# Kernel tuning notes

Hardware: AMD Instinct MI355X
Metric: run time of the kernel (lower is better)

Reference implementation:

```python
import jax, jax.numpy as jnp
import numpy as np

B, S, E, N, H = 2, 2048, 2048, 16, 128  # batch, seq, embed, heads, depth


def sine_table(features, length, min_timescale=1.0, max_timescale=10000.0):
    fraction = jnp.arange(0, features, 2, dtype=jnp.float32) / features
    timescale = min_timescale * (max_timescale / min_timescale) ** fraction
    sinusoid_inp = jnp.einsum('i,j->ij', jnp.arange(length, dtype=jnp.float32), 1.0 / timescale,
                              precision=jax.lax.Precision.HIGHEST)
    sinusoid_inp = jnp.concatenate([sinusoid_inp, sinusoid_inp], axis=-1)  # [L, features]
    return jnp.sin(sinusoid_inp), jnp.cos(sinusoid_inp)


def rotate_half(x):
    x1, x2 = jnp.split(x, 2, axis=-1)
    return jnp.concatenate([-x2, x1], axis=-1)


def apply_rotary(q, k, cos, sin):
    # q: [B,S,N,H], k: [B,T,N,H]; cos/sin: [L,H] broadcast over (seq, depth)
    qcos = cos[: q.shape[1]][None, :, None, :]
    qsin = sin[: q.shape[1]][None, :, None, :]
    kcos = cos[: k.shape[1]][None, :, None, :]
    ksin = sin[: k.shape[1]][None, :, None, :]
    return q * qcos + rotate_half(q) * qsin, k * kcos + rotate_half(k) * ksin


def setup_inputs() -> dict:
    key = jax.random.key(0)
    ks = jax.random.split(key, 6)
    scale = 1.0 / np.sqrt(E)
    return {
        'x_q': jax.random.normal(ks[0], (B, S, E), jnp.float32),
        'x_kv': jax.random.normal(ks[1], (B, S, E), jnp.float32),
        'WQ': jax.random.normal(ks[2], (E, N, H), jnp.float32) * scale,
        'WK': jax.random.normal(ks[3], (E, N, H), jnp.float32) * scale,
        'WV': jax.random.normal(ks[4], (E, N, H), jnp.float32) * scale,
        'WO': jax.random.normal(ks[5], (N, H, E), jnp.float32) * scale,
    }


def reference(x_q, x_kv, WQ, WK, WV, WO):
    q = jnp.einsum('bse,enh->bsnh', x_q, WQ)
    k = jnp.einsum('bte,enh->btnh', x_kv, WK)
    v = jnp.einsum('bte,enh->btnh', x_kv, WV)

    sin, cos = sine_table(q.shape[-1], max(q.shape[1], k.shape[1]))
    q, k = apply_rotary(q, k, cos, sin)

    # causal attention bias: [1,1,S,T]
    s_len, t_len = q.shape[1], k.shape[1]
    causal = jnp.arange(s_len)[:, None] >= jnp.arange(t_len)[None, :]
    bias = jnp.where(causal, 0.0, -1e10).astype(jnp.float32)[None, None]

    logits = jnp.einsum('bsnh,btnh->bnst', q, k) / np.sqrt(H) + bias
    probs = jax.nn.softmax(logits, axis=-1)
    a = jnp.einsum('bnst,btnh->bsnh', probs, v)
    o = jnp.einsum('bsnh,nhe->bse', a, WO)
    return o
```

## Files before the change

### kernel.cpp

```cpp
#include <hip/hip_runtime.h>
#include <hip/hip_bf16.h>

typedef __bf16 bf16;
typedef __attribute__((ext_vector_type(8))) __bf16 bf16x8;
typedef __attribute__((ext_vector_type(4))) __bf16 bf16x4;
typedef __attribute__((ext_vector_type(4))) float f32x4;

typedef const __attribute__((address_space(1))) void* gptr_t;
typedef __attribute__((address_space(3))) void* sptr_t;

__device__ __forceinline__ void gload16(const void* g, void* l) {
  __builtin_amdgcn_global_load_lds((gptr_t)g, (sptr_t)l, 16, 0, 0);
}

#define MFMA_BF16(a, b, c) __builtin_amdgcn_mfma_f32_16x16x32_bf16((a), (b), (c), 0, 0, 0)

#define BAR() do { asm volatile("" ::: "memory"); __builtin_amdgcn_s_barrier(); asm volatile("" ::: "memory"); } while (0)

__device__ __forceinline__ int swzb(int l) { return l ^ (((l >> 7) & 7) << 4); }

namespace {
constexpr int kB = 2, kS = 2048, kE = 2048, kN = 16, kH = 128;
constexpr float kScale = 0.08838834764831845f;
constexpr float kLog2e = 1.4426950408889634f;
}

__global__ void k_cvt(const float* __restrict__ in, bf16* __restrict__ out) {
  int i = blockIdx.x * 256 + threadIdx.x;
  float4 v = reinterpret_cast<const float4*>(in)[i];
  bf16x4 o = { (bf16)v.x, (bf16)v.y, (bf16)v.z, (bf16)v.w };
  reinterpret_cast<bf16x4*>(out)[i] = o;
}

__global__ void k_tconv(const float* __restrict__ in, bf16* __restrict__ out) {
  __shared__ bf16 tile[64][66];
  int bx = blockIdx.x & 31, by = blockIdx.x >> 5;
  int r0 = by * 64, c0 = bx * 64;
  int t = threadIdx.x;
  int c = t & 63, rb = t >> 6;
#pragma unroll
  for (int j = 0; j < 16; ++j) {
    int r = rb + j * 4;
    tile[r][c] = (bf16)in[(size_t)(r0 + r) * 2048 + c0 + c];
  }
  __syncthreads();
  int rr = t & 63;
#pragma unroll
  for (int j = 0; j < 16; ++j) {
    int cc = rb + j * 4;
    out[(size_t)(c0 + cc) * 2048 + r0 + rr] = tile[rr][cc];
  }
}

__global__ void k_vtrans(const bf16* __restrict__ V, bf16* __restrict__ Vt) {
  __shared__ bf16 tile[64][66];
  int bid = blockIdx.x;
  int bn = bid >> 6;
  int s0 = ((bid >> 1) & 31) * 64;
  int h0 = (bid & 1) * 64;
  size_t base = (size_t)bn * kS * kH;
  int t = threadIdx.x, c = t & 63, rb = t >> 6;
#pragma unroll
  for (int j = 0; j < 16; ++j) {
    int r = rb + j * 4;
    tile[r][c] = V[base + (size_t)(s0 + r) * kH + h0 + c];
  }
  __syncthreads();
#pragma unroll
  for (int j = 0; j < 16; ++j) {
    int hh = rb + j * 4;
    Vt[base + (size_t)(h0 + hh) * kS + s0 + (t & 63)] = tile[t & 63][hh];
  }
}

__global__ void k_trig(float* __restrict__ ctab, float* __restrict__ stab) {
  int tid = blockIdx.x * 256 + threadIdx.x;
  int s = tid >> 6, i = tid & 63;
  float inv = exp2f(-(float)i * 0.20762050593046457f);
  float ang = (float)s * inv;
  float sn, cs;
  sincosf(ang, &sn, &cs);
  ctab[tid] = cs;
  stab[tid] = sn;
}

__global__ void k_rope(bf16* __restrict__ Qd, bf16* __restrict__ Kd,
                       const float* __restrict__ ctab, const float* __restrict__ stab) {
  int tid = blockIdx.x * 256 + threadIdx.x;
  int i = tid & 63;
  int s = (tid >> 6) & (kS - 1);
  int bn = tid >> 17;
  size_t base = ((size_t)bn * kS + s) * kH;
  float cs = ctab[(s << 6) + i], sn = stab[(s << 6) + i];
  float q1 = (float)Qd[base + i], q2 = (float)Qd[base + i + 64];
  Qd[base + i]      = (bf16)(q1 * cs - q2 * sn);
  Qd[base + i + 64] = (bf16)(q2 * cs + q1 * sn);
  float k1 = (float)Kd[base + i], k2 = (float)Kd[base + i + 64];
  Kd[base + i]      = (bf16)(k1 * cs - k2 * sn);
  Kd[base + i + 64] = (bf16)(k2 * cs + k1 * sn);
}


__device__ __forceinline__ void stage_half(const bf16* __restrict__ src, size_t row0,
                                           int k0, char* slot, int t) {
#pragma unroll
  for (int i = 0; i < 2; ++i) {
    int idx = i * 512 + t;
    int d = idx * 16;
    int lb = d ^ (((d >> 7) & 7) << 4);
    int r = lb >> 7;
    int kc = (lb & 127) >> 1;
    gload16(src + (row0 + r) * 2048 + k0 + kc,
            slot + i * 8192 + (t >> 6) * 1024);
  }
}

#define ASB(b, h) ((char*)LDS + (b) * 32768 + (h) * 16384)
#define BSB(b, h) ((char*)LDS + 65536 + (b) * 32768 + (h) * 16384)
#define AS1(b)    ((char*)LDS + (b) * 16384)
#define BS1(q, h) ((char*)LDS + 32768 + (q) * 32768 + (h) * 16384)

template <int MODE>
__global__ __launch_bounds__(512, 2) void k_gemm8(const bf16* __restrict__ Aq,
                                                  const bf16* __restrict__ Akv,
                                                  const bf16* __restrict__ Bt,
                                                  void* __restrict__ Cout) {
  constexpr int NTN = (MODE == 0) ? 24 : 8;
  constexpr int NTM = (MODE == 0) ? 16 : 32;
  constexpr int NT = 32;
  constexpr int BM = (MODE == 0) ? 256 : 128;
  __shared__ __align__(16) char LDS[131072];
  int bid = blockIdx.x;
  constexpr int nblk = NTM * NTN;
  int swz = (bid & 7) * (nblk >> 3) + (bid >> 3);
  int mt = swz / NTN, nt = swz - mt * NTN;
  size_t m0 = (size_t)mt * BM;
  int n0 = nt * 256;
  const bf16* A = (MODE == 0 && nt >= 8) ? Akv : Aq;
  int t = threadIdx.x, wid = t >> 6, lane = t & 63;
  int l16 = lane & 15, lq = lane >> 4;
  int wr = wid >> 2, wc = wid & 3;
  int bhalf = wc >> 1;
  int brow0 = ((wc & 1) << 6) + l16;

  constexpr int MF = (MODE == 0) ? 8 : 4;
  f32x4 acc[MF][4] = {};
  bf16x8 af[4], bfr[4];

  if constexpr (MODE == 0) {
    stage_half(Bt, (size_t)n0,       0, BSB(0, 0), t);
    stage_half(Bt, (size_t)n0 + 128, 0, BSB(0, 1), t);
    stage_half(A,  m0,               0, ASB(0, 0), t);
    stage_half(A,  m0 + 128,         0, ASB(0, 1), t);
    stage_half(Bt, (size_t)n0,      64, BSB(1, 0), t);
    stage_half(Bt, (size_t)n0 + 128, 64, BSB(1, 1), t);
    asm volatile("s_waitcnt vmcnt(4)" ::: "memory");
    BAR();

    for (int kt = 0; kt < NT; ++kt) {
      int buf = kt & 1, nbuf = buf ^ 1;
#pragma unroll
      for (int j = 0; j < 4; ++j) {
        int l = ((j * 16 + l16) << 7) + (lq << 4);
        af[j] = *(const bf16x8*)(ASB(buf, wr) + swzb(l));
      }
#pragma unroll
      for (int nf = 0; nf < 4; ++nf) {
        int l = ((brow0 + nf * 16) << 7) + (lq << 4);
        bfr[nf] = *(const bf16x8*)(BSB(buf, bhalf) + swzb(l));
      }
      if (kt + 1 < NT) stage_half(A, m0, (kt + 1) * 64, ASB(nbuf, 0), t);
      BAR();
      __builtin_amdgcn_s_setprio(1);
#pragma unroll
      for (int j = 0; j < 4; ++j)
#pragma unroll
        for (int nf = 0; nf < 4; ++nf)
          acc[j][nf] = MFMA_BF16(af[j], bfr[nf], acc[j][nf]);
      __builtin_amdgcn_s_setprio(0);
      BAR();
#pragma unroll
      for (int j = 0; j < 4; ++j) {
        int l = (((j + 4) * 16 + l16) << 7) + (lq << 4);
        af[j] = *(const bf16x8*)(ASB(buf, wr) + swzb(l));
      }
      if (kt + 1 < NT) stage_half(A, m0 + 128, (kt + 1) * 64, ASB(nbuf, 1), t);
      BAR();
      __builtin_amdgcn_s_setprio(1);
#pragma unroll
      for (int j = 0; j < 4; ++j)
#pragma unroll
        for (int nf = 0; nf < 4; ++nf)
          acc[j + 4][nf] = MFMA_BF16(af[j], bfr[nf], acc[j + 4][nf]);
      __builtin_amdgcn_s_setprio(0);
      BAR();
#pragma unroll
      for (int j = 0; j < 4; ++j) {
        int l = ((j * 16 + l16) << 7) + 64 + (lq << 4);
        af[j] = *(const bf16x8*)(ASB(buf, wr) + swzb(l));
      }
#pragma unroll
      for (int nf = 0; nf < 4; ++nf) {
        int l = ((brow0 + nf * 16) << 7) + 64 + (lq << 4);
        bfr[nf] = *(const bf16x8*)(BSB(buf, bhalf) + swzb(l));
      }
      BAR();
      __builtin_amdgcn_s_setprio(1);
#pragma unroll
      for (int j = 0; j < 4; ++j)
#pragma unroll
        for (int nf = 0; nf < 4; ++nf)
          acc[j][nf] = MFMA_BF16(af[j], bfr[nf], acc[j][nf]);
      __builtin_amdgcn_s_setprio(0);
      BAR();
#pragma unroll
      for (int j = 0; j < 4; ++j) {
        int l = (((j + 4) * 16 + l16) << 7) + 64 + (lq << 4);
        af[j] = *(const bf16x8*)(ASB(buf, wr) + swzb(l));
      }
      if (kt + 2 < NT) {
        stage_half(Bt, (size_t)n0,       (kt + 2) * 64, BSB(buf, 0), t);
        stage_half(Bt, (size_t)n0 + 128, (kt + 2) * 64, BSB(buf, 1), t);
      }
      BAR();
      __builtin_amdgcn_s_setprio(1);
#pragma unroll
      for (int j = 0; j < 4; ++j)
#pragma unroll
        for (int nf = 0; nf < 4; ++nf)
          acc[j + 4][nf] = MFMA_BF16(af[j], bfr[nf], acc[j + 4][nf]);
      __builtin_amdgcn_s_setprio(0);
      if (kt < NT - 2)       asm volatile("s_waitcnt vmcnt(4)" ::: "memory");
      else if (kt == NT - 2) asm volatile("s_waitcnt vmcnt(0)" ::: "memory");
      BAR();
    }
  } else {
    stage_half(Bt, (size_t)n0,       0, BS1(0, 0), t);
    stage_half(Bt, (size_t)n0 + 128, 0, BS1(0, 1), t);
    stage_half(A,  m0,               0, AS1(0), t);
    stage_half(Bt, (size_t)n0,      64, BS1(1, 0), t);
    stage_half(Bt, (size_t)n0 + 128, 64, BS1(1, 1), t);
    asm volatile("s_waitcnt vmcnt(4)" ::: "memory");
    BAR();

    int bql = 0;
    for (int kt = 0; kt < NT; ++kt) {
      char* Ab = AS1(kt & 1);
      char* Anb = AS1((kt & 1) ^ 1);
      char* Bb = BS1(bql, bhalf);
      int bq2 = bql + 2; if (bq2 >= 3) bq2 -= 3;
#pragma unroll
      for (int j = 0; j < 4; ++j) {
        int l = (((wr * 4 + j) * 16 + l16) << 7) + (lq << 4);
        af[j] = *(const bf16x8*)(Ab + swzb(l));
      }
#pragma unroll
      for (int nf = 0; nf < 2; ++nf) {
        int l = ((brow0 + nf * 16) << 7) + (lq << 4);
        bfr[nf] = *(const bf16x8*)(Bb + swzb(l));
      }
      if (kt + 1 < NT) stage_half(A, m0, (kt + 1) * 64, Anb, t);
      BAR();
      __builtin_amdgcn_s_setprio(1);
#pragma unroll
      for (int j = 0; j < 4; ++j)
#pragma unroll
        for (int nf = 0; nf < 2; ++nf)
          acc[j][nf] = MFMA_BF16(af[j], bfr[nf], acc[j][nf]);
      __builtin_amdgcn_s_setprio(0);
      BAR();
#pragma unroll
      for (int nf = 0; nf < 2; ++nf) {
        int l = ((brow0 + (nf + 2) * 16) << 7) + (lq << 4);
        bfr[2 + nf] = *(const bf16x8*)(Bb + swzb(l));
      }
      if (kt + 2 < NT) {
        stage_half(Bt, (size_t)n0,       (kt + 2) * 64, BS1(bq2, 0), t);
        stage_half(Bt, (size_t)n0 + 128, (kt + 2) * 64, BS1(bq2, 1), t);
      }
      BAR();
      __builtin_amdgcn_s_setprio(1);
#pragma unroll
      for (int j = 0; j < 4; ++j)
#pragma unroll
        for (int nf = 0; nf < 2; ++nf)
          acc[j][2 + nf] = MFMA_BF16(af[j], bfr[2 + nf], acc[j][2 + nf]);
      __builtin_amdgcn_s_setprio(0);
      BAR();
#pragma unroll
      for (int j = 0; j < 4; ++j) {
        int l = (((wr * 4 + j) * 16 + l16) << 7) + 64 + (lq << 4);
        af[j] = *(const bf16x8*)(Ab + swzb(l));
      }
#pragma unroll
      for (int nf = 0; nf < 2; ++nf) {
        int l = ((brow0 + nf * 16) << 7) + 64 + (lq << 4);
        bfr[nf] = *(const bf16x8*)(Bb + swzb(l));
      }
      BAR();
      __builtin_amdgcn_s_setprio(1);
#pragma unroll
      for (int j = 0; j < 4; ++j)
#pragma unroll
        for (int nf = 0; nf < 2; ++nf)
          acc[j][nf] = MFMA_BF16(af[j], bfr[nf], acc[j][nf]);
      __builtin_amdgcn_s_setprio(0);
      BAR();
#pragma unroll
      for (int nf = 0; nf < 2; ++nf) {
        int l = ((brow0 + (nf + 2) * 16) << 7) + 64 + (lq << 4);
        bfr[2 + nf] = *(const bf16x8*)(Bb + swzb(l));
      }
      BAR();
      __builtin_amdgcn_s_setprio(1);
#pragma unroll
      for (int j = 0; j < 4; ++j)
#pragma unroll
        for (int nf = 0; nf < 2; ++nf)
          acc[j][2 + nf] = MFMA_BF16(af[j], bfr[2 + nf], acc[j][2 + nf]);
      __builtin_amdgcn_s_setprio(0);
      if (kt < NT - 2)       asm volatile("s_waitcnt vmcnt(4)" ::: "memory");
      else if (kt == NT - 2) asm volatile("s_waitcnt vmcnt(0)" ::: "memory");
      BAR();
      bql += 1; if (bql >= 3) bql -= 3;
    }
  }

  constexpr int WRS = (MODE == 0) ? 128 : 64;
#pragma unroll
  for (int mf = 0; mf < MF; ++mf) {
    int rowb = (int)m0 + wr * WRS + mf * 16 + lq * 4;
#pragma unroll
    for (int nf = 0; nf < 4; ++nf) {
      int col = n0 + wc * 64 + nf * 16 + l16;
#pragma unroll
      for (int r = 0; r < 4; ++r) {
        float v = acc[mf][nf][r];
        int mrow = rowb + r;
        if (MODE == 0) {
          int grp = col >> 11, cw = col & 2047;
          int b = mrow >> 11, s = mrow & 2047, n = cw >> 7, h = cw & 127;
          ((bf16*)Cout)[(size_t)grp * 8388608 +
                        (((size_t)(b * 16 + n) * 2048 + s) << 7) + h] = (bf16)v;
        } else {
          ((float*)Cout)[((size_t)mrow << 11) + col] = v;
        }
      }
    }
  }
}

__global__ __launch_bounds__(512, 4) void k_attn(const bf16* __restrict__ Q,
                                                 const bf16* __restrict__ Kg,
                                                 const bf16* __restrict__ Vt,
                                                 bf16* __restrict__ AO) {
  __shared__ __align__(16) bf16 Ks[64 * 128];
  __shared__ __align__(16) bf16 Vs[128 * 64];
  __shared__ __align__(16) bf16 Ps[8][16][72];
  int bid = blockIdx.x;
  int half = bid >> 8;
  int bn = (half << 4) | ((bid >> 4) & 15);
  int qt = (bid & 15) ^ (half ? 15 : 0);
  int q0 = qt * 128;
  int t = threadIdx.x, wid = t >> 6, lane = t & 63;
  int l16 = lane & 15, lq = lane >> 4;
  size_t bnSH = (size_t)bn * kS * kH;

  int qrow_a = q0 + wid * 16 + l16;
  bf16x8 qf[4];
#pragma unroll
  for (int ks = 0; ks < 4; ++ks)
    qf[ks] = *(const bf16x8*)(Q + bnSH + (size_t)qrow_a * kH + ks * 32 + lq * 8);

  f32x4 oacc[8] = {};
  float mrun[4], lrun[4];
#pragma unroll
  for (int r = 0; r < 4; ++r) { mrun[r] = -1e30f; lrun[r] = 0.f; }

  int ntiles = (q0 + 128) >> 6;
  for (int kt = 0; kt < ntiles; ++kt) {
    int kv0 = kt * 64;
#pragma unroll
    for (int i = 0; i < 2; ++i) {
      int idx = i * 512 + t;
      {
        int row = idx >> 4, ch = idx & 15;
        int gch = ch ^ (row & 7);
        gload16(Kg + bnSH + (size_t)(kv0 + row) * kH + gch * 8,
                (char*)Ks + i * 8192 + wid * 1024);
      }
      {
        int row = idx >> 3, ch = idx & 7;
        int gch = ch ^ (row & 7);
        gload16(Vt + bnSH + (size_t)row * kS + kv0 + gch * 8,
                (char*)Vs + i * 8192 + wid * 1024);
      }
    }
    __syncthreads();

    f32x4 sacc[4] = {};
#pragma unroll
    for (int ks = 0; ks < 4; ++ks) {
#pragma unroll
      for (int ni = 0; ni < 4; ++ni) {
        int sp = ni * 16 + l16;
        int hb = (ks * 32 + lq * 8) * 2;
        bf16x8 kb = *(const bf16x8*)((const char*)Ks + sp * 256 + (hb ^ ((sp & 7) << 4)));
        sacc[ni] = MFMA_BF16(qf[ks], kb, sacc[ni]);
      }
    }

    bool need_mask = (kv0 + 63) > (q0 + wid * 16);
#pragma unroll
    for (int ni = 0; ni < 4; ++ni) {
      f32x4 v = sacc[ni] * kScale;
      if (need_mask) {
#pragma unroll
        for (int r = 0; r < 4; ++r) {
          int qrow = q0 + wid * 16 + lq * 4 + r;
          int col = kv0 + ni * 16 + l16;
          if (col > qrow) v[r] = -1e30f;
        }
      }
      sacc[ni] = v;
    }

#pragma unroll
    for (int r = 0; r < 4; ++r) {
      float pm = fmaxf(fmaxf(sacc[0][r], sacc[1][r]),
                       fmaxf(sacc[2][r], sacc[3][r]));
      pm = fmaxf(pm, __shfl_xor(pm, 1));
      pm = fmaxf(pm, __shfl_xor(pm, 2));
      pm = fmaxf(pm, __shfl_xor(pm, 4));
      pm = fmaxf(pm, __shfl_xor(pm, 8));
      float mold = mrun[r];
      float mnew = fmaxf(mold, pm);
      float alpha = exp2f((mold - mnew) * kLog2e);
      mrun[r] = mnew;
      float rs = 0.f;
#pragma unroll
      for (int ni = 0; ni < 4; ++ni) {
        float p = exp2f((sacc[ni][r] - mnew) * kLog2e);
        sacc[ni][r] = p;
        rs += p;
      }
      rs += __shfl_xor(rs, 1);
      rs += __shfl_xor(rs, 2);
      rs += __shfl_xor(rs, 4);
      rs += __shfl_xor(rs, 8);
      lrun[r] = lrun[r] * alpha + rs;
#pragma unroll
      for (int nj = 0; nj < 8; ++nj) oacc[nj][r] *= alpha;
    }

#pragma unroll
    for (int ni = 0; ni < 4; ++ni)
#pragma unroll
      for (int r = 0; r < 4; ++r)
        Ps[wid][lq * 4 + r][ni * 16 + l16] = (bf16)sacc[ni][r];

#pragma unroll
    for (int ks = 0; ks < 2; ++ks) {
      bf16x8 pa = *(const bf16x8*)&Ps[wid][l16][ks * 32 + lq * 8];
#pragma unroll
      for (int nj = 0; nj < 8; ++nj) {
        int h = nj * 16 + l16;
        int sb = (ks * 64 + lq * 16) ^ ((h & 7) << 4);
        bf16x8 vb = *(const bf16x8*)((const char*)Vs + h * 128 + sb);
        oacc[nj] = MFMA_BF16(pa, vb, oacc[nj]);
      }
    }
    __syncthreads();
  }

  int b = bn >> 4, n = bn & 15;
#pragma unroll
  for (int r = 0; r < 4; ++r) {
    float inv = 1.0f / lrun[r];
    int qrow = q0 + wid * 16 + lq * 4 + r;
#pragma unroll
    for (int nj = 0; nj < 8; ++nj) {
      float v = oacc[nj][r] * inv;
      AO[(((size_t)b * kS + qrow) * kN + n) * kH + nj * 16 + l16] = (bf16)v;
    }
  }
}

extern "C" void kernel_launch(void* const* d_in, const int* in_sizes, int n_in,
                              void* d_out, int out_size, void* d_ws, size_t ws_size,
                              hipStream_t stream) {
  (void)in_sizes; (void)n_in; (void)out_size; (void)ws_size;
  const float* x_q  = (const float*)d_in[0];
  const float* x_kv = (const float*)d_in[1];
  const float* WQ   = (const float*)d_in[2];
  const float* WK   = (const float*)d_in[3];
  const float* WV   = (const float*)d_in[4];
  const float* WO   = (const float*)d_in[5];
  float* out = (float*)d_out;
  char* w = (char*)d_ws;
  const size_t MB = 1ull << 20;
  bf16* xq  = (bf16*)(w + 0 * MB);
  bf16* xkv = (bf16*)(w + 16 * MB);
  bf16* WqT = (bf16*)(w + 32 * MB);
  bf16* WkT = (bf16*)(w + 40 * MB);
  bf16* WvT = (bf16*)(w + 48 * MB);
  bf16* WoT = (bf16*)(w + 56 * MB);
  bf16* Qb  = (bf16*)(w + 64 * MB);
  bf16* Kb  = (bf16*)(w + 80 * MB);
  bf16* Vb  = (bf16*)(w + 96 * MB);
  float* ctab = (float*)(w + 0 * MB);
  float* stab = (float*)(w + 1 * MB);
  bf16* AO  = xq;
  bf16* Vtb = xkv;

  k_cvt<<<8192, 256, 0, stream>>>(x_q, xq);
  k_cvt<<<8192, 256, 0, stream>>>(x_kv, xkv);
  k_tconv<<<1024, 256, 0, stream>>>(WQ, WqT);
  k_tconv<<<1024, 256, 0, stream>>>(WK, WkT);
  k_tconv<<<1024, 256, 0, stream>>>(WV, WvT);
  k_tconv<<<1024, 256, 0, stream>>>(WO, WoT);
  k_gemm8<0><<<384, 512, 0, stream>>>(xq, xkv, WqT, Qb);
  k_trig<<<512, 256, 0, stream>>>(ctab, stab);
  k_rope<<<16384, 256, 0, stream>>>(Qb, Kb, ctab, stab);
  k_vtrans<<<2048, 256, 0, stream>>>(Vb, Vtb);
  k_attn<<<512, 512, 0, stream>>>(Qb, Kb, Vtb, AO);
  k_gemm8<1><<<256, 512, 0, stream>>>(AO, AO, WoT, out);
}
```

Baseline: 447.6 us.

## Merge prep kernels, vectorize transposes and rope, unify GEMM to 128-row tiles

Two conversion launches become one, and the four weight-transpose launches become one. The transpose, V-transpose and rope kernels now use 8-wide bf16 and float4 vector loads and stores in place of scalar element accesses. The QKV projection GEMM drops its 256-row tile path and reuses the 128-row triple-buffered-B path with twice as many blocks. The attention P staging buffer gets an XOR swizzle in place of padding, to avoid LDS bank conflicts. These changes aim to cut launch overhead and memory-instruction count, at the cost of more A-tile reloads per B tile in the projection GEMM.

```diff
diff --git a/kernel.cpp b/kernel.cpp
--- a/kernel.cpp
+++ b/kernel.cpp
@@ -25,51 +25,73 @@
 constexpr float kLog2e = 1.4426950408889634f;
 }
 
-__global__ void k_cvt(const float* __restrict__ in, bf16* __restrict__ out) {
-  int i = blockIdx.x * 256 + threadIdx.x;
+__global__ void k_cvt2(const float* __restrict__ a, const float* __restrict__ b,
+                       bf16* __restrict__ oa, bf16* __restrict__ ob) {
+  int bid = blockIdx.x;
+  const float* in = (bid < 8192) ? a : b;
+  bf16* out = (bid < 8192) ? oa : ob;
+  int i = (bid & 8191) * 256 + threadIdx.x;
   float4 v = reinterpret_cast<const float4*>(in)[i];
   bf16x4 o = { (bf16)v.x, (bf16)v.y, (bf16)v.z, (bf16)v.w };
   reinterpret_cast<bf16x4*>(out)[i] = o;
 }
 
-__global__ void k_tconv(const float* __restrict__ in, bf16* __restrict__ out) {
-  __shared__ bf16 tile[64][66];
-  int bx = blockIdx.x & 31, by = blockIdx.x >> 5;
+__global__ void k_tconv4(const float* __restrict__ WQ, const float* __restrict__ WK,
+                         const float* __restrict__ WV, const float* __restrict__ WO,
+                         bf16* __restrict__ OQ, bf16* __restrict__ OK2,
+                         bf16* __restrict__ OV, bf16* __restrict__ OO) {
+  __shared__ float tile[64][68];
+  int bid = blockIdx.x;
+  int sel = bid >> 10;
+  const float* in = (sel == 0) ? WQ : (sel == 1) ? WK : (sel == 2) ? WV : WO;
+  bf16* out = (sel == 0) ? OQ : (sel == 1) ? OK2 : (sel == 2) ? OV : OO;
+  int lb = bid & 1023;
+  int bx = lb & 31, by = lb >> 5;
   int r0 = by * 64, c0 = bx * 64;
   int t = threadIdx.x;
-  int c = t & 63, rb = t >> 6;
-#pragma unroll
-  for (int j = 0; j < 16; ++j) {
-    int r = rb + j * 4;
-    tile[r][c] = (bf16)in[(size_t)(r0 + r) * 2048 + c0 + c];
+  int rr = t >> 4, c4 = (t & 15) * 4;
+#pragma unroll
+  for (int k = 0; k < 4; ++k) {
+    int r = rr + k * 16;
+    float4 v = *reinterpret_cast<const float4*>(&in[(size_t)(r0 + r) * 2048 + c0 + c4]);
+    tile[r][c4] = v.x; tile[r][c4 + 1] = v.y; tile[r][c4 + 2] = v.z; tile[r][c4 + 3] = v.w;
   }
   __syncthreads();
-  int rr = t & 63;
-#pragma unroll
-  for (int j = 0; j < 16; ++j) {
-    int cc = rb + j * 4;
-    out[(size_t)(c0 + cc) * 2048 + r0 + rr] = tile[rr][cc];
+  int cc0 = t >> 3, r8 = (t & 7) * 8;
+#pragma unroll
+  for (int k = 0; k < 2; ++k) {
+    int cc = cc0 + k * 32;
+    bf16x8 o;
+#pragma unroll
+    for (int j = 0; j < 8; ++j) o[j] = (bf16)tile[r8 + j][cc];
+    *reinterpret_cast<bf16x8*>(&out[(size_t)(c0 + cc) * 2048 + r0 + r8]) = o;
   }
 }
 
 __global__ void k_vtrans(const bf16* __restrict__ V, bf16* __restrict__ Vt) {
-  __shared__ bf16 tile[64][66];
+  __shared__ bf16 tile[64][72];
   int bid = blockIdx.x;
   int bn = bid >> 6;
   int s0 = ((bid >> 1) & 31) * 64;
   int h0 = (bid & 1) * 64;
   size_t base = (size_t)bn * kS * kH;
-  int t = threadIdx.x, c = t & 63, rb = t >> 6;
-#pragma unroll
-  for (int j = 0; j < 16; ++j) {
-    int r = rb + j * 4;
-    tile[r][c] = V[base + (size_t)(s0 + r) * kH + h0 + c];
+  int t = threadIdx.x;
+  int r = t >> 3, c8 = (t & 7) * 8;
+#pragma unroll
+  for (int k = 0; k < 2; ++k) {
+    int rr = r + k * 32;
+    *reinterpret_cast<bf16x8*>(&tile[rr][c8]) =
+        *reinterpret_cast<const bf16x8*>(&V[base + (size_t)(s0 + rr) * kH + h0 + c8]);
   }
   __syncthreads();
-#pragma unroll
-  for (int j = 0; j < 16; ++j) {
-    int hh = rb + j * 4;
-    Vt[base + (size_t)(h0 + hh) * kS + s0 + (t & 63)] = tile[t & 63][hh];
+  int hh0 = t >> 3, s8 = (t & 7) * 8;
+#pragma unroll
+  for (int k = 0; k < 2; ++k) {
+    int hh = hh0 + k * 32;
+    bf16x8 o;
+#pragma unroll
+    for (int j = 0; j < 8; ++j) o[j] = tile[s8 + j][hh];
+    *reinterpret_cast<bf16x8*>(&Vt[base + (size_t)(h0 + hh) * kS + s0 + s8]) = o;
   }
 }
 
@@ -87,17 +109,34 @@
 __global__ void k_rope(bf16* __restrict__ Qd, bf16* __restrict__ Kd,
                        const float* __restrict__ ctab, const float* __restrict__ stab) {
   int tid = blockIdx.x * 256 + threadIdx.x;
-  int i = tid & 63;
-  int s = (tid >> 6) & (kS - 1);
-  int bn = tid >> 17;
+  int i8 = (tid & 7) * 8;
+  int s = (tid >> 3) & (kS - 1);
+  int bn = tid >> 14;
   size_t base = ((size_t)bn * kS + s) * kH;
-  float cs = ctab[(s << 6) + i], sn = stab[(s << 6) + i];
-  float q1 = (float)Qd[base + i], q2 = (float)Qd[base + i + 64];
-  Qd[base + i]      = (bf16)(q1 * cs - q2 * sn);
-  Qd[base + i + 64] = (bf16)(q2 * cs + q1 * sn);
-  float k1 = (float)Kd[base + i], k2 = (float)Kd[base + i + 64];
-  Kd[base + i]      = (bf16)(k1 * cs - k2 * sn);
-  Kd[base + i + 64] = (bf16)(k2 * cs + k1 * sn);
+  float4 c0 = *reinterpret_cast<const float4*>(&ctab[(s << 6) + i8]);
+  float4 c1 = *reinterpret_cast<const float4*>(&ctab[(s << 6) + i8 + 4]);
+  float4 s0 = *reinterpret_cast<const float4*>(&stab[(s << 6) + i8]);
+  float4 s1 = *reinterpret_cast<const float4*>(&stab[(s << 6) + i8 + 4]);
+  float cs[8] = {c0.x, c0.y, c0.z, c0.w, c1.x, c1.y, c1.z, c1.w};
+  float sn[8] = {s0.x, s0.y, s0.z, s0.w, s1.x, s1.y, s1.z, s1.w};
+  bf16x8 qlo = *reinterpret_cast<const bf16x8*>(&Qd[base + i8]);
+  bf16x8 qhi = *reinterpret_cast<const bf16x8*>(&Qd[base + 64 + i8]);
+  bf16x8 klo = *reinterpret_cast<const bf16x8*>(&Kd[base + i8]);
+  bf16x8 khi = *reinterpret_cast<const bf16x8*>(&Kd[base + 64 + i8]);
+  bf16x8 qlo2, qhi2, klo2, khi2;
+#pragma unroll
+  for (int j = 0; j < 8; ++j) {
+    float q1 = (float)qlo[j], q2 = (float)qhi[j];
+    qlo2[j] = (bf16)(q1 * cs[j] - q2 * sn[j]);
+    qhi2[j] = (bf16)(q2 * cs[j] + q1 * sn[j]);
+    float k1 = (float)klo[j], k2 = (float)khi[j];
+    klo2[j] = (bf16)(k1 * cs[j] - k2 * sn[j]);
+    khi2[j] = (bf16)(k2 * cs[j] + k1 * sn[j]);
+  }
+  *reinterpret_cast<bf16x8*>(&Qd[base + i8]) = qlo2;
+  *reinterpret_cast<bf16x8*>(&Qd[base + 64 + i8]) = qhi2;
+  *reinterpret_cast<bf16x8*>(&Kd[base + i8]) = klo2;
+  *reinterpret_cast<bf16x8*>(&Kd[base + 64 + i8]) = khi2;
 }
 
 
@@ -115,8 +154,6 @@
   }
 }
 
-#define ASB(b, h) ((char*)LDS + (b) * 32768 + (h) * 16384)
-#define BSB(b, h) ((char*)LDS + 65536 + (b) * 32768 + (h) * 16384)
 #define AS1(b)    ((char*)LDS + (b) * 16384)
 #define BS1(q, h) ((char*)LDS + 32768 + (q) * 32768 + (h) * 16384)
 
@@ -126,15 +163,14 @@
                                                   const bf16* __restrict__ Bt,
                                                   void* __restrict__ Cout) {
   constexpr int NTN = (MODE == 0) ? 24 : 8;
-  constexpr int NTM = (MODE == 0) ? 16 : 32;
+  constexpr int NTM = 32;
   constexpr int NT = 32;
-  constexpr int BM = (MODE == 0) ? 256 : 128;
   __shared__ __align__(16) char LDS[131072];
   int bid = blockIdx.x;
   constexpr int nblk = NTM * NTN;
   int swz = (bid & 7) * (nblk >> 3) + (bid >> 3);
   int mt = swz / NTN, nt = swz - mt * NTN;
-  size_t m0 = (size_t)mt * BM;
+  size_t m0 = (size_t)mt * 128;
   int n0 = nt * 256;
   const bf16* A = (MODE == 0 && nt >= 8) ? Akv : Aq;
   int t = threadIdx.x, wid = t >> 6, lane = t & 63;
@@ -143,193 +179,102 @@
   int bhalf = wc >> 1;
   int brow0 = ((wc & 1) << 6) + l16;
 
-  constexpr int MF = (MODE == 0) ? 8 : 4;
-  f32x4 acc[MF][4] = {};
+  f32x4 acc[4][4] = {};
   bf16x8 af[4], bfr[4];
 
-  if constexpr (MODE == 0) {
-    stage_half(Bt, (size_t)n0,       0, BSB(0, 0), t);
-    stage_half(Bt, (size_t)n0 + 128, 0, BSB(0, 1), t);
-    stage_half(A,  m0,               0, ASB(0, 0), t);
-    stage_half(A,  m0 + 128,         0, ASB(0, 1), t);
-    stage_half(Bt, (size_t)n0,      64, BSB(1, 0), t);
-    stage_half(Bt, (size_t)n0 + 128, 64, BSB(1, 1), t);
-    asm volatile("s_waitcnt vmcnt(4)" ::: "memory");
-    BAR();
-
-    for (int kt = 0; kt < NT; ++kt) {
-      int buf = kt & 1, nbuf = buf ^ 1;
-#pragma unroll
-      for (int j = 0; j < 4; ++j) {
-        int l = ((j * 16 + l16) << 7) + (lq << 4);
-        af[j] = *(const bf16x8*)(ASB(buf, wr) + swzb(l));
-      }
-#pragma unroll
-      for (int nf = 0; nf < 4; ++nf) {
-        int l = ((brow0 + nf * 16) << 7) + (lq << 4);
-        bfr[nf] = *(const bf16x8*)(BSB(buf, bhalf) + swzb(l));
-      }
-      if (kt + 1 < NT) stage_half(A, m0, (kt + 1) * 64, ASB(nbuf, 0), t);
-      BAR();
-      __builtin_amdgcn_s_setprio(1);
-#pragma unroll
-      for (int j = 0; j < 4; ++j)
-#pragma unroll
-        for (int nf = 0; nf < 4; ++nf)
-          acc[j][nf] = MFMA_BF16(af[j], bfr[nf], acc[j][nf]);
-      __builtin_amdgcn_s_setprio(0);
-      BAR();
-#pragma unroll
-      for (int j = 0; j < 4; ++j) {
-        int l = (((j + 4) * 16 + l16) << 7) + (lq << 4);
-        af[j] = *(const bf16x8*)(ASB(buf, wr) + swzb(l));
-      }
-      if (kt + 1 < NT) stage_half(A, m0 + 128, (kt + 1) * 64, ASB(nbuf, 1), t);
-      BAR();
-      __builtin_amdgcn_s_setprio(1);
-#pragma unroll
-      for (int j = 0; j < 4; ++j)
-#pragma unroll
-        for (int nf = 0; nf < 4; ++nf)
-          acc[j + 4][nf] = MFMA_BF16(af[j], bfr[nf], acc[j + 4][nf]);
-      __builtin_amdgcn_s_setprio(0);
-      BAR();
-#pragma unroll
-      for (int j = 0; j < 4; ++j) {
-        int l = ((j * 16 + l16) << 7) + 64 + (lq << 4);
-        af[j] = *(const bf16x8*)(ASB(buf, wr) + swzb(l));
-      }
-#pragma unroll
-      for (int nf = 0; nf < 4; ++nf) {
-        int l = ((brow0 + nf * 16) << 7) + 64 + (lq << 4);
-        bfr[nf] = *(const bf16x8*)(BSB(buf, bhalf) + swzb(l));
-      }
-      BAR();
-      __builtin_amdgcn_s_setprio(1);
-#pragma unroll
-      for (int j = 0; j < 4; ++j)
-#pragma unroll
-        for (int nf = 0; nf < 4; ++nf)
-          acc[j][nf] = MFMA_BF16(af[j], bfr[nf], acc[j][nf]);
-      __builtin_amdgcn_s_setprio(0);
-      BAR();
-#pragma unroll
-      for (int j = 0; j < 4; ++j) {
-        int l = (((j + 4) * 16 + l16) << 7) + 64 + (lq << 4);
-        af[j] = *(const bf16x8*)(ASB(buf, wr) + swzb(l));
-      }
-      if (kt + 2 < NT) {
-        stage_half(Bt, (size_t)n0,       (kt + 2) * 64, BSB(buf, 0), t);
-        stage_half(Bt, (size_t)n0 + 128, (kt + 2) * 64, BSB(buf, 1), t);
-      }
-      BAR();
-      __builtin_amdgcn_s_setprio(1);
-#pragma unroll
-      for (int j = 0; j < 4; ++j)
-#pragma unroll
-        for (int nf = 0; nf < 4; ++nf)
-          acc[j + 4][nf] = MFMA_BF16(af[j], bfr[nf], acc[j + 4][nf]);
-      __builtin_amdgcn_s_setprio(0);
-      if (kt < NT - 2)       asm volatile("s_waitcnt vmcnt(4)" ::: "memory");
-      else if (kt == NT - 2) asm volatile("s_waitcnt vmcnt(0)" ::: "memory");
-      BAR();
-    }
-  } else {
-    stage_half(Bt, (size_t)n0,       0, BS1(0, 0), t);
-    stage_half(Bt, (size_t)n0 + 128, 0, BS1(0, 1), t);
-    stage_half(A,  m0,               0, AS1(0), t);
-    stage_half(Bt, (size_t)n0,      64, BS1(1, 0), t);
-    stage_half(Bt, (size_t)n0 + 128, 64, BS1(1, 1), t);
-    asm volatile("s_waitcnt vmcnt(4)" ::: "memory");
-    BAR();
-
-    int bql = 0;
-    for (int kt = 0; kt < NT; ++kt) {
-      char* Ab = AS1(kt & 1);
-      char* Anb = AS1((kt & 1) ^ 1);
-      char* Bb = BS1(bql, bhalf);
-      int bq2 = bql + 2; if (bq2 >= 3) bq2 -= 3;
-#pragma unroll
-      for (int j = 0; j < 4; ++j) {
-        int l = (((wr * 4 + j) * 16 + l16) << 7) + (lq << 4);
-        af[j] = *(const bf16x8*)(Ab + swzb(l));
-      }
-#pragma unroll
-      for (int nf = 0; nf < 2; ++nf) {
-        int l = ((brow0 + nf * 16) << 7) + (lq << 4);
-        bfr[nf] = *(const bf16x8*)(Bb + swzb(l));
-      }
-      if (kt + 1 < NT) stage_half(A, m0, (kt + 1) * 64, Anb, t);
-      BAR();
-      __builtin_amdgcn_s_setprio(1);
-#pragma unroll
-      for (int j = 0; j < 4; ++j)
-#pragma unroll
-        for (int nf = 0; nf < 2; ++nf)
-          acc[j][nf] = MFMA_BF16(af[j], bfr[nf], acc[j][nf]);
-      __builtin_amdgcn_s_setprio(0);
-      BAR();
-#pragma unroll
-      for (int nf = 0; nf < 2; ++nf) {
-        int l = ((brow0 + (nf + 2) * 16) << 7) + (lq << 4);
-        bfr[2 + nf] = *(const bf16x8*)(Bb + swzb(l));
-      }
-      if (kt + 2 < NT) {
-        stage_half(Bt, (size_t)n0,       (kt + 2) * 64, BS1(bq2, 0), t);
-        stage_half(Bt, (size_t)n0 + 128, (kt + 2) * 64, BS1(bq2, 1), t);
-      }
-      BAR();
-      __builtin_amdgcn_s_setprio(1);
-#pragma unroll
-      for (int j = 0; j < 4; ++j)
-#pragma unroll
-        for (int nf = 0; nf < 2; ++nf)
-          acc[j][2 + nf] = MFMA_BF16(af[j], bfr[2 + nf], acc[j][2 + nf]);
-      __builtin_amdgcn_s_setprio(0);
-      BAR();
-#pragma unroll
-      for (int j = 0; j < 4; ++j) {
-        int l = (((wr * 4 + j) * 16 + l16) << 7) + 64 + (lq << 4);
-        af[j] = *(const bf16x8*)(Ab + swzb(l));
-      }
-#pragma unroll
-      for (int nf = 0; nf < 2; ++nf) {
-        int l = ((brow0 + nf * 16) << 7) + 64 + (lq << 4);
-        bfr[nf] = *(const bf16x8*)(Bb + swzb(l));
-      }
-      BAR();
-      __builtin_amdgcn_s_setprio(1);
-#pragma unroll
-      for (int j = 0; j < 4; ++j)
-#pragma unroll
-        for (int nf = 0; nf < 2; ++nf)
-          acc[j][nf] = MFMA_BF16(af[j], bfr[nf], acc[j][nf]);
-      __builtin_amdgcn_s_setprio(0);
-      BAR();
-#pragma unroll
-      for (int nf = 0; nf < 2; ++nf) {
-        int l = ((brow0 + (nf + 2) * 16) << 7) + 64 + (lq << 4);
-        bfr[2 + nf] = *(const bf16x8*)(Bb + swzb(l));
-      }
-      BAR();
-      __builtin_amdgcn_s_setprio(1);
-#pragma unroll
-      for (int j = 0; j < 4; ++j)
-#pragma unroll
-        for (int nf = 0; nf < 2; ++nf)
-          acc[j][2 + nf] = MFMA_BF16(af[j], bfr[2 + nf], acc[j][2 + nf]);
-      __builtin_amdgcn_s_setprio(0);
-      if (kt < NT - 2)       asm volatile("s_waitcnt vmcnt(4)" ::: "memory");
-      else if (kt == NT - 2) asm volatile("s_waitcnt vmcnt(0)" ::: "memory");
-      BAR();
-      bql += 1; if (bql >= 3) bql -= 3;
-    }
-  }
-
-  constexpr int WRS = (MODE == 0) ? 128 : 64;
-#pragma unroll
-  for (int mf = 0; mf < MF; ++mf) {
-    int rowb = (int)m0 + wr * WRS + mf * 16 + lq * 4;
+  stage_half(Bt, (size_t)n0,       0, BS1(0, 0), t);
+  stage_half(Bt, (size_t)n0 + 128, 0, BS1(0, 1), t);
+  stage_half(A,  m0,               0, AS1(0), t);
+  stage_half(Bt, (size_t)n0,      64, BS1(1, 0), t);
+  stage_half(Bt, (size_t)n0 + 128, 64, BS1(1, 1), t);
+  asm volatile("s_waitcnt vmcnt(4)" ::: "memory");
+  BAR();
+
+  int bql = 0;
+  for (int kt = 0; kt < NT; ++kt) {
+    char* Ab = AS1(kt & 1);
+    char* Anb = AS1((kt & 1) ^ 1);
+    char* Bb = BS1(bql, bhalf);
+    int bq2 = bql + 2; if (bq2 >= 3) bq2 -= 3;
+#pragma unroll
+    for (int j = 0; j < 4; ++j) {
+      int l = (((wr * 4 + j) * 16 + l16) << 7) + (lq << 4);
+      af[j] = *(const bf16x8*)(Ab + swzb(l));
+    }
+#pragma unroll
+    for (int nf = 0; nf < 2; ++nf) {
+      int l = ((brow0 + nf * 16) << 7) + (lq << 4);
+      bfr[nf] = *(const bf16x8*)(Bb + swzb(l));
+    }
+    if (kt + 1 < NT) stage_half(A, m0, (kt + 1) * 64, Anb, t);
+    BAR();
+    __builtin_amdgcn_s_setprio(1);
+#pragma unroll
+    for (int j = 0; j < 4; ++j)
+#pragma unroll
+      for (int nf = 0; nf < 2; ++nf)
+        acc[j][nf] = MFMA_BF16(af[j], bfr[nf], acc[j][nf]);
+    __builtin_amdgcn_s_setprio(0);
+    BAR();
+#pragma unroll
+    for (int nf = 0; nf < 2; ++nf) {
+      int l = ((brow0 + (nf + 2) * 16) << 7) + (lq << 4);
+      bfr[2 + nf] = *(const bf16x8*)(Bb + swzb(l));
+    }
+    if (kt + 2 < NT) {
+      stage_half(Bt, (size_t)n0,       (kt + 2) * 64, BS1(bq2, 0), t);
+      stage_half(Bt, (size_t)n0 + 128, (kt + 2) * 64, BS1(bq2, 1), t);
+    }
+    BAR();
+    __builtin_amdgcn_s_setprio(1);
+#pragma unroll
+    for (int j = 0; j < 4; ++j)
+#pragma unroll
+      for (int nf = 0; nf < 2; ++nf)
+        acc[j][2 + nf] = MFMA_BF16(af[j], bfr[2 + nf], acc[j][2 + nf]);
+    __builtin_amdgcn_s_setprio(0);
+    BAR();
+#pragma unroll
+    for (int j = 0; j < 4; ++j) {
+      int l = (((wr * 4 + j) * 16 + l16) << 7) + 64 + (lq << 4);
+      af[j] = *(const bf16x8*)(Ab + swzb(l));
+    }
+#pragma unroll
+    for (int nf = 0; nf < 2; ++nf) {
+      int l = ((brow0 + nf * 16) << 7) + 64 + (lq << 4);
+      bfr[nf] = *(const bf16x8*)(Bb + swzb(l));
+    }
+    BAR();
+    __builtin_amdgcn_s_setprio(1);
+#pragma unroll
+    for (int j = 0; j < 4; ++j)
+#pragma unroll
+      for (int nf = 0; nf < 2; ++nf)
+        acc[j][nf] = MFMA_BF16(af[j], bfr[nf], acc[j][nf]);
+    __builtin_amdgcn_s_setprio(0);
+    BAR();
+#pragma unroll
+    for (int nf = 0; nf < 2; ++nf) {
+      int l = ((brow0 + (nf + 2) * 16) << 7) + 64 + (lq << 4);
+      bfr[2 + nf] = *(const bf16x8*)(Bb + swzb(l));
+    }
+    BAR();
+    __builtin_amdgcn_s_setprio(1);
+#pragma unroll
+    for (int j = 0; j < 4; ++j)
+#pragma unroll
+      for (int nf = 0; nf < 2; ++nf)
+        acc[j][2 + nf] = MFMA_BF16(af[j], bfr[2 + nf], acc[j][2 + nf]);
+    __builtin_amdgcn_s_setprio(0);
+    if (kt < NT - 2)       asm volatile("s_waitcnt vmcnt(4)" ::: "memory");
+    else if (kt == NT - 2) asm volatile("s_waitcnt vmcnt(0)" ::: "memory");
+    BAR();
+    bql += 1; if (bql >= 3) bql -= 3;
+  }
+
+#pragma unroll
+  for (int mf = 0; mf < 4; ++mf) {
+    int rowb = (int)m0 + wr * 64 + mf * 16 + lq * 4;
 #pragma unroll
     for (int nf = 0; nf < 4; ++nf) {
       int col = n0 + wc * 64 + nf * 16 + l16;
@@ -356,7 +301,7 @@
                                                  bf16* __restrict__ AO) {
   __shared__ __align__(16) bf16 Ks[64 * 128];
   __shared__ __align__(16) bf16 Vs[128 * 64];
-  __shared__ __align__(16) bf16 Ps[8][16][72];
+  __shared__ __align__(16) bf16 Ps[8 * 16 * 64];
   int bid = blockIdx.x;
   int half = bid >> 8;
   int bn = (half << 4) | ((bid >> 4) & 15);
@@ -456,12 +401,16 @@
 #pragma unroll
     for (int ni = 0; ni < 4; ++ni)
 #pragma unroll
-      for (int r = 0; r < 4; ++r)
-        Ps[wid][lq * 4 + r][ni * 16 + l16] = (bf16)sacc[ni][r];
+      for (int r = 0; r < 4; ++r) {
+        int row = lq * 4 + r;
+        int byte = (row << 7) + ((ni * 16 + l16) << 1);
+        *(bf16*)((char*)Ps + wid * 2048 + (byte ^ ((row & 7) << 4))) = (bf16)sacc[ni][r];
+      }
 
 #pragma unroll
     for (int ks = 0; ks < 2; ++ks) {
-      bf16x8 pa = *(const bf16x8*)&Ps[wid][l16][ks * 32 + lq * 8];
+      int pb = (l16 << 7) + ((ks * 64 + lq * 16) ^ ((l16 & 7) << 4));
+      bf16x8 pa = *(const bf16x8*)((const char*)Ps + wid * 2048 + pb);
 #pragma unroll
       for (int nj = 0; nj < 8; ++nj) {
         int h = nj * 16 + l16;
@@ -513,15 +462,11 @@
   bf16* AO  = xq;
   bf16* Vtb = xkv;
 
-  k_cvt<<<8192, 256, 0, stream>>>(x_q, xq);
-  k_cvt<<<8192, 256, 0, stream>>>(x_kv, xkv);
-  k_tconv<<<1024, 256, 0, stream>>>(WQ, WqT);
-  k_tconv<<<1024, 256, 0, stream>>>(WK, WkT);
-  k_tconv<<<1024, 256, 0, stream>>>(WV, WvT);
-  k_tconv<<<1024, 256, 0, stream>>>(WO, WoT);
-  k_gemm8<0><<<384, 512, 0, stream>>>(xq, xkv, WqT, Qb);
+  k_cvt2<<<16384, 256, 0, stream>>>(x_q, x_kv, xq, xkv);
+  k_tconv4<<<4096, 256, 0, stream>>>(WQ, WK, WV, WO, WqT, WkT, WvT, WoT);
+  k_gemm8<0><<<768, 512, 0, stream>>>(xq, xkv, WqT, Qb);
   k_trig<<<512, 256, 0, stream>>>(ctab, stab);
-  k_rope<<<16384, 256, 0, stream>>>(Qb, Kb, ctab, stab);
+  k_rope<<<2048, 256, 0, stream>>>(Qb, Kb, ctab, stab);
   k_vtrans<<<2048, 256, 0, stream>>>(Vb, Vtb);
   k_attn<<<512, 512, 0, stream>>>(Qb, Kb, Vtb, AO);
   k_gemm8<1><<<256, 512, 0, stream>>>(AO, AO, WoT, out);
```

Measured after the change: 460.2 us. +2.8%, slower.
